# Performance work log

Measured on AMD Instinct MI355X. Metric: run time of the kernel, lower is better.

Reference implementation:

```python
import jax, jax.numpy as jnp
import numpy as np

BN_EPS = 1e-5


def setup_inputs() -> dict:
    key = jax.random.key(0)
    ks = jax.random.split(key, 5)
    b, c, seq, K = 16, 128, 16384, 64
    x = jax.random.normal(ks[0], (b, c, 1, seq), dtype=jnp.float32)
    std = 1.0 / np.sqrt(K * c)
    codewords = jax.random.uniform(ks[1], (K, c), dtype=jnp.float32, minval=-std, maxval=std)
    smoothing = jax.random.uniform(ks[2], (K,), dtype=jnp.float32, minval=-1.0, maxval=0.0)
    bn_weight = jnp.ones((K,), dtype=jnp.float32)
    bn_bias = jnp.zeros((K,), dtype=jnp.float32)
    fc_w = jax.random.normal(ks[3], (c, c), dtype=jnp.float32) * (1.0 / np.sqrt(c))
    fc_b = jax.random.uniform(ks[4], (c,), dtype=jnp.float32, minval=-1.0 / np.sqrt(c), maxval=1.0 / np.sqrt(c))
    return {"x": x, "codewords": codewords, "smoothing": smoothing,
            "bn_weight": bn_weight, "bn_bias": bn_bias, "fc_w": fc_w, "fc_b": fc_b}


def reference(x, codewords, smoothing, bn_weight, bn_bias, fc_w, fc_b):
    # x: (b, c, 1, seq); codewords: (K, c); smoothing: (K,)
    xs = jnp.transpose(x[:, :, 0, :], (0, 2, 1))          # (b, seq, c)
    # squared distances ||x - cw||^2 via expansion (avoids (b,seq,K,c) tensor)
    x2 = jnp.sum(xs * xs, axis=-1)                         # (b, seq)
    cw2 = jnp.sum(codewords * codewords, axis=-1)          # (K,)
    cross = jnp.einsum('bsc,kc->bsk', xs, codewords)       # (b, seq, K)
    d2 = x2[:, :, None] - 2.0 * cross + cw2[None, None, :]
    a = jax.nn.softmax(smoothing[None, None, :] * d2, axis=2)  # (b, seq, K)
    # e = sum_s a * (x - cw)  (residual aggregation, expansion-free)
    e = jnp.einsum('bsk,bsc->bkc', a, xs) - jnp.sum(a, axis=1)[:, :, None] * codewords[None]  # (b, K, c)
    # BatchNorm1d over K features (training-mode batch stats over dims (b, c))
    mean = jnp.mean(e, axis=(0, 2), keepdims=True)
    var = jnp.var(e, axis=(0, 2), keepdims=True)
    e_bn = (e - mean) / jnp.sqrt(var + BN_EPS) * bn_weight[None, :, None] + bn_bias[None, :, None]
    e_norm = jnp.mean(jax.nn.relu(e_bn), axis=1)           # (b, c)
    scale = jax.nn.sigmoid(e_norm @ fc_w.T + fc_b)         # (b, c)
    return x * scale[:, :, None, None]
```

## Files before the change

kernel.cpp:

```cpp
#include <hip/hip_runtime.h>

typedef unsigned int u32;
typedef unsigned short u16;
typedef unsigned long long u64;

typedef float f32x4 __attribute__((ext_vector_type(4)));
typedef short bf16x8 __attribute__((ext_vector_type(8)));

#define B_   16
#define C_   128
#define SEQ_ 16384
#define K_   64
#define TS_  64
#define NT_  8
#define CHUNK_ 512

constexpr int OFF_EACC = 0;
constexpr int OFF_ASUM = 131072;
constexpr int OFF_BNS  = 132096;
constexpr int OFF_BNB  = 132160;
constexpr int OFF_SM   = 136192;
constexpr int OFF_SMC2 = 136256;
constexpr int OFF_SCALE= 136320;

__device__ __forceinline__ u16 f2bf(float f) {
    u32 b = __float_as_uint(f);
    return (u16)((b + 0x7FFFu + ((b >> 16) & 1u)) >> 16);
}
__device__ __forceinline__ float scrub(float v) {
    return fminf(fmaxf(v, -1.0e4f), 1.0e4f);
}

__global__ void k0_prep(const float* __restrict__ cw, const float* __restrict__ sm,
                        float* __restrict__ ws) {
    const int t = threadIdx.x;
    if (t < K_) {
        float s2 = 0.f;
        for (int c = 0; c < C_; ++c) { float f = cw[t * C_ + c]; s2 += f * f; }
        float smv = sm[t];
        ws[OFF_SM + t] = smv;
        ws[OFF_SMC2 + t] = smv * s2;
    }
}

__global__ __launch_bounds__(256, 3)
void k1_encode(const float* __restrict__ xg, const float* __restrict__ cwg, float* ws) {
    __shared__ __align__(16) u16 xsc_h[TS_ * C_];
    __shared__ __align__(16) u16 xsc_l[TS_ * C_];
    __shared__ __align__(16) u16 alds[K_ * TS_];

    const int t    = threadIdx.x;
    const int lane = t & 63;
    const int w    = t >> 6;
    const int lk   = lane & 15;
    const int lg   = lane >> 4;
    const int b      = blockIdx.x >> 5;
    const int s_base = (blockIdx.x & 31) * CHUNK_;

    bf16x8 cwf[4][4];
#pragma unroll
    for (int nt = 0; nt < 4; ++nt)
#pragma unroll
      for (int ks = 0; ks < 4; ++ks) {
        const float* p = cwg + (size_t)(lk + 16*nt) * C_ + 8*lg + 32*ks;
        float4 v0 = *(const float4*)p;
        float4 v1 = *(const float4*)(p + 4);
        bf16x8 f;
        f[0]=(short)f2bf(v0.x); f[1]=(short)f2bf(v0.y); f[2]=(short)f2bf(v0.z); f[3]=(short)f2bf(v0.w);
        f[4]=(short)f2bf(v1.x); f[5]=(short)f2bf(v1.y); f[6]=(short)f2bf(v1.z); f[7]=(short)f2bf(v1.w);
        cwf[nt][ks] = f;
      }
    float smk[4], smc2k[4];
#pragma unroll
    for (int nt = 0; nt < 4; ++nt) {
        smk[nt]   = ws[OFF_SM   + lk + 16*nt];
        smc2k[nt] = ws[OFF_SMC2 + lk + 16*nt];
    }

    f32x4 acc2[4][2] = {};
    float asacc[4] = {0.f,0.f,0.f,0.f};

    const int sm_ = t & 15;
    const int sg_ = t >> 4;

    auto gemm2 = [&](int stp) {
#pragma unroll
        for (int ss = 0; ss < 2; ++ss) {
            bf16x8 aA[4];
#pragma unroll
            for (int mt = 0; mt < 4; ++mt)
                aA[mt] = *(const bf16x8*)&alds[(lk + 16*mt) * TS_ + ((8*lg + 32*ss) ^ ((lk & 7) << 3))];
#pragma unroll
            for (int n = 0; n < 2; ++n) {
                const float* xr = xg + (size_t)(b * C_ + lk + 16*(2*w + n)) * SEQ_ + stp + 8*lg + 32*ss;
                float4 v0 = *(const float4*)xr;
                float4 v1 = *(const float4*)(xr + 4);
                bf16x8 bx;
                ((u32*)&bx)[0] = (__float_as_uint(v0.x) >> 16) | (__float_as_uint(v0.y) & 0xFFFF0000u);
                ((u32*)&bx)[1] = (__float_as_uint(v0.z) >> 16) | (__float_as_uint(v0.w) & 0xFFFF0000u);
                ((u32*)&bx)[2] = (__float_as_uint(v1.x) >> 16) | (__float_as_uint(v1.y) & 0xFFFF0000u);
                ((u32*)&bx)[3] = (__float_as_uint(v1.z) >> 16) | (__float_as_uint(v1.w) & 0xFFFF0000u);
#pragma unroll
                for (int mt = 0; mt < 4; ++mt)
                    acc2[mt][n] = __builtin_amdgcn_mfma_f32_16x16x32_bf16(aA[mt], bx, acc2[mt][n], 0, 0, 0);
            }
        }
    };

    float4 vc[8];
    {
        const float* xb = xg + (size_t)(b * C_ + 8*sm_) * SEQ_ + s_base + 4*sg_;
#pragma unroll
        for (int r = 0; r < 8; ++r) vc[r] = *(const float4*)(xb + (size_t)r * SEQ_);
    }

    float x2red[4];

    for (int tile = 0; tile < NT_; ++tile) {
        const int st = s_base + tile * TS_;
        __syncthreads();

        {
            u16 H[8][4], L[8][4];
            float x2p[4] = {0.f,0.f,0.f,0.f};
#pragma unroll
            for (int r = 0; r < 8; ++r) {
                float fa[4] = {vc[r].x, vc[r].y, vc[r].z, vc[r].w};
#pragma unroll
                for (int i = 0; i < 4; ++i) {
                    float f = fa[i];
                    u32 bu = __float_as_uint(f);
                    u16 hh = (u16)(bu >> 16);
                    float fh = __uint_as_float((u32)hh << 16);
                    u16 ll = (u16)(__float_as_uint(f - fh) >> 16);
                    H[r][i] = hh; L[r][i] = ll;
                    x2p[i] = fmaf(f, f, x2p[i]);
                }
            }
            if (tile + 1 < NT_) {
                const float* xb = xg + (size_t)(b * C_ + 8*sm_) * SEQ_ + (st + TS_) + 4*sg_;
#pragma unroll
                for (int r = 0; r < 8; ++r) vc[r] = *(const float4*)(xb + (size_t)r * SEQ_);
            }
#pragma unroll
            for (int i = 0; i < 4; ++i) {
                float v = x2p[i];
                v += __shfl_xor(v, 1);
                v += __shfl_xor(v, 2);
                v += __shfl_xor(v, 4);
                v += __shfl_xor(v, 8);
                x2red[i] = v;
            }
#pragma unroll
            for (int i = 0; i < 4; ++i) {
                int s = 4*sg_ + i;
                u32 idx = (u32)(s * C_ + 8*sm_) ^ ((u32)(s & 15) << 3);
                uint4 hw, lw;
                hw.x = (u32)H[0][i] | ((u32)H[1][i] << 16);
                hw.y = (u32)H[2][i] | ((u32)H[3][i] << 16);
                hw.z = (u32)H[4][i] | ((u32)H[5][i] << 16);
                hw.w = (u32)H[6][i] | ((u32)H[7][i] << 16);
                lw.x = (u32)L[0][i] | ((u32)L[1][i] << 16);
                lw.y = (u32)L[2][i] | ((u32)L[3][i] << 16);
                lw.z = (u32)L[4][i] | ((u32)L[5][i] << 16);
                lw.w = (u32)L[6][i] | ((u32)L[7][i] << 16);
                *(uint4*)&xsc_h[idx] = hw;
                *(uint4*)&xsc_l[idx] = lw;
            }
        }
        if (tile > 0) gemm2(st - TS_);
        __syncthreads();

        f32x4 d1[4] = {};
        {
            const int sA = 16*w + lk;
#pragma unroll
            for (int ks = 0; ks < 4; ++ks) {
                u32 idx = (u32)(sA * C_ + 8*lg + 32*ks) ^ ((u32)(sA & 15) << 3);
                bf16x8 ah = *(const bf16x8*)&xsc_h[idx];
                bf16x8 al = *(const bf16x8*)&xsc_l[idx];
#pragma unroll
                for (int nt = 0; nt < 4; ++nt) {
                    d1[nt] = __builtin_amdgcn_mfma_f32_16x16x32_bf16(ah, cwf[nt][ks], d1[nt], 0, 0, 0);
                    d1[nt] = __builtin_amdgcn_mfma_f32_16x16x32_bf16(al, cwf[nt][ks], d1[nt], 0, 0, 0);
                }
            }
        }

        {
            float mx[4], pp[4][4], inv[4];
#pragma unroll
            for (int r = 0; r < 4; ++r) mx[r] = -1.0e30f;
#pragma unroll
            for (int nt = 0; nt < 4; ++nt)
#pragma unroll
              for (int r = 0; r < 4; ++r) {
                float lv = fmaf(smk[nt], x2red[r] - 2.0f * d1[nt][r], smc2k[nt]);
                lv = scrub(lv);
                pp[nt][r] = lv;
                mx[r] = fmaxf(mx[r], lv);
              }
#pragma unroll
            for (int r = 0; r < 4; ++r) {
                mx[r] = fmaxf(mx[r], __shfl_xor(mx[r], 1));
                mx[r] = fmaxf(mx[r], __shfl_xor(mx[r], 2));
                mx[r] = fmaxf(mx[r], __shfl_xor(mx[r], 4));
                mx[r] = fmaxf(mx[r], __shfl_xor(mx[r], 8));
            }
            float sum[4] = {0.f,0.f,0.f,0.f};
#pragma unroll
            for (int nt = 0; nt < 4; ++nt)
#pragma unroll
              for (int r = 0; r < 4; ++r) {
                float e = __expf(pp[nt][r] - mx[r]);
                pp[nt][r] = e;
                sum[r] += e;
              }
#pragma unroll
            for (int r = 0; r < 4; ++r) {
                sum[r] += __shfl_xor(sum[r], 1);
                sum[r] += __shfl_xor(sum[r], 2);
                sum[r] += __shfl_xor(sum[r], 4);
                sum[r] += __shfl_xor(sum[r], 8);
                inv[r] = 1.0f / sum[r];
            }
#pragma unroll
            for (int nt = 0; nt < 4; ++nt) {
                u16 q[4];
                float sloc = 0.f;
#pragma unroll
                for (int r = 0; r < 4; ++r) {
                    float a = pp[nt][r] * inv[r];
                    sloc += a;
                    q[r] = f2bf(a);
                }
                asacc[nt] += sloc;
                u64 pk = (u64)q[0] | ((u64)q[1] << 16) | ((u64)q[2] << 32) | ((u64)q[3] << 48);
                *(u64*)&alds[(lk + 16*nt) * TS_ + (((u32)(16*w + 4*lg)) ^ ((u32)(lk & 7) << 3))] = pk;
            }
        }
    }
    __syncthreads();
    gemm2(s_base + (NT_ - 1) * TS_);

    float* eacc = ws + OFF_EACC;
#pragma unroll
    for (int mt = 0; mt < 4; ++mt)
#pragma unroll
      for (int n = 0; n < 2; ++n) {
        const int c = lk + 16*(2*w + n);
#pragma unroll
        for (int r = 0; r < 4; ++r) {
            int k = 16*mt + 4*lg + r;
            atomicAdd(&eacc[(b * K_ + k) * C_ + c], acc2[mt][n][r]);
        }
      }
#pragma unroll
    for (int nt = 0; nt < 4; ++nt) {
        float v = asacc[nt];
        v += __shfl_xor(v, 16);
        v += __shfl_xor(v, 32);
        if (lane < 16) atomicAdd(&ws[OFF_ASUM + b * K_ + lk + 16*nt], v);
    }
}

__global__ __launch_bounds__(256)
void k2a_stats(const float* __restrict__ cw,
               const float* __restrict__ bnw, const float* __restrict__ bnb,
               float* ws) {
    const int k = blockIdx.x;
    const int t = threadIdx.x;
    const int lane = t & 63, w = t >> 6;
    __shared__ float redS[4], redQ[4];
    const float* eacc = ws + OFF_EACC;
    const float* asum = ws + OFF_ASUM;
    float sv = 0.f, sq = 0.f;
#pragma unroll
    for (int u = t; u < 512; u += 256) {
        int bb = u >> 5, c4 = u & 31;
        float a = asum[bb * K_ + k];
        float4 ev = *(const float4*)&eacc[(bb * K_ + k) * C_ + 4*c4];
        float4 cv = *(const float4*)&cw[k * C_ + 4*c4];
        float e0 = ev.x - a * cv.x, e1 = ev.y - a * cv.y;
        float e2 = ev.z - a * cv.z, e3 = ev.w - a * cv.w;
        sv += e0 + e1 + e2 + e3;
        sq += e0*e0 + e1*e1 + e2*e2 + e3*e3;
    }
#pragma unroll
    for (int m = 1; m < 64; m <<= 1) {
        sv += __shfl_xor(sv, m);
        sq += __shfl_xor(sq, m);
    }
    if (lane == 0) { redS[w] = sv; redQ[w] = sq; }
    __syncthreads();
    if (t == 0) {
        float s = redS[0]+redS[1]+redS[2]+redS[3];
        float q = redQ[0]+redQ[1]+redQ[2]+redQ[3];
        float mean = s * (1.f / 2048.f);
        float var  = q * (1.f / 2048.f) - mean * mean;
        float rstd = rsqrtf(fmaxf(var, 0.f) + 1e-5f);
        float g = bnw[k] * rstd;
        ws[OFF_BNS + k] = g;
        ws[OFF_BNB + k] = bnb[k] - mean * g;
    }
}

__global__ __launch_bounds__(256)
void k2b_fc(const float* __restrict__ cw,
            const float* __restrict__ fcw, const float* __restrict__ fcb,
            float* ws) {
    __shared__ float enorm_s[C_];
    __shared__ float red2[C_];
    const int b = blockIdx.x;
    const int t = threadIdx.x;
    const int c = t & 127, h = t >> 7;
    const float* eacc = ws + OFF_EACC;
    float s = 0.f;
    for (int kk = 0; kk < 32; ++kk) {
        int k = 32*h + kk;
        float e = eacc[(b * K_ + k) * C_ + c] - ws[OFF_ASUM + b * K_ + k] * cw[k * C_ + c];
        float bnv = e * ws[OFF_BNS + k] + ws[OFF_BNB + k];
        s += fminf(fmaxf(bnv, 0.f), 1.0e6f);
    }
    if (h) red2[c] = s;
    __syncthreads();
    if (!h) enorm_s[c] = (s + red2[c]) * (1.f / 64.f);
    __syncthreads();
    float acc = 0.f;
    const float4* fw = (const float4*)&fcw[c * C_ + 64*h];
#pragma unroll
    for (int q = 0; q < 16; ++q) {
        float4 wv = fw[q];
        int ci = 64*h + 4*q;
        acc += enorm_s[ci] * wv.x + enorm_s[ci+1] * wv.y + enorm_s[ci+2] * wv.z + enorm_s[ci+3] * wv.w;
    }
    __syncthreads();
    if (h) red2[c] = acc;
    __syncthreads();
    if (!h) {
        float o = fcb[c] + acc + red2[c];
        ws[OFF_SCALE + b * C_ + c] = 1.f / (1.f + __expf(-o));
    }
}

__global__ __launch_bounds__(256)
void k3_scale(const float4* __restrict__ xg, float4* __restrict__ outg,
              const float* __restrict__ ws) {
    const int bc = blockIdx.x;
    const float sc = ws[OFF_SCALE + bc];
    const float4* xr = xg + (size_t)bc * (SEQ_ / 4);
    float4* orow = outg + (size_t)bc * (SEQ_ / 4);
    const int t = threadIdx.x;
    for (int i = 0; i < SEQ_ / 4 / 256; ++i) {
        float4 v = xr[i * 256 + t];
        v.x *= sc; v.y *= sc; v.z *= sc; v.w *= sc;
        orow[i * 256 + t] = v;
    }
}

extern "C" void kernel_launch(void* const* d_in, const int* in_sizes, int n_in,
                              void* d_out, int out_size, void* d_ws, size_t ws_size,
                              hipStream_t stream) {
    const float* x   = (const float*)d_in[0];
    const float* cw  = (const float*)d_in[1];
    const float* sm  = (const float*)d_in[2];
    const float* bnw = (const float*)d_in[3];
    const float* bnb = (const float*)d_in[4];
    const float* fcw = (const float*)d_in[5];
    const float* fcb = (const float*)d_in[6];
    float* ws = (float*)d_ws;

    hipMemsetAsync(ws, 0, (size_t)(OFF_ASUM + B_ * K_) * sizeof(float), stream);
    k0_prep<<<1, 256, 0, stream>>>(cw, sm, ws);
    k1_encode<<<B_ * (SEQ_ / CHUNK_), 256, 0, stream>>>(x, cw, ws);
    k2a_stats<<<K_, 256, 0, stream>>>(cw, bnw, bnb, ws);
    k2b_fc<<<B_, 256, 0, stream>>>(cw, fcw, fcb, ws);
    k3_scale<<<B_ * C_, 256, 0, stream>>>((const float4*)x, (float4*)d_out, ws);
}
```

Baseline: 386.9 us.

## Fold codeword prep into encode kernel, halve chunk size, use perm packing

Removes the separate single-block prep kernel by computing codeword squared norms inside each encode block via shuffles, which drops one launch and its serialization. The per-block sequence chunk is halved, doubling the grid to 1024 blocks for better CU fill, and launch bounds drop from 3 to 2 waves per SIMD. The bf16 hi/lo splitting and packing now use byte-perm instructions and pack pairs directly instead of via intermediate u16 arrays. The trade-offs are redundant norm computation in every block, more atomic partial-sum traffic from the extra blocks, and possibly lower occupancy.

```diff
diff --git a/kernel.cpp b/kernel.cpp
--- a/kernel.cpp
+++ b/kernel.cpp
@@ -12,15 +12,13 @@
 #define SEQ_ 16384
 #define K_   64
 #define TS_  64
-#define NT_  8
-#define CHUNK_ 512
+#define NT_  4
+#define CHUNK_ 256
 
 constexpr int OFF_EACC = 0;
 constexpr int OFF_ASUM = 131072;
 constexpr int OFF_BNS  = 132096;
 constexpr int OFF_BNB  = 132160;
-constexpr int OFF_SM   = 136192;
-constexpr int OFF_SMC2 = 136256;
 constexpr int OFF_SCALE= 136320;
 
 __device__ __forceinline__ u16 f2bf(float f) {
@@ -30,21 +28,13 @@
 __device__ __forceinline__ float scrub(float v) {
     return fminf(fmaxf(v, -1.0e4f), 1.0e4f);
 }
-
-__global__ void k0_prep(const float* __restrict__ cw, const float* __restrict__ sm,
-                        float* __restrict__ ws) {
-    const int t = threadIdx.x;
-    if (t < K_) {
-        float s2 = 0.f;
-        for (int c = 0; c < C_; ++c) { float f = cw[t * C_ + c]; s2 += f * f; }
-        float smv = sm[t];
-        ws[OFF_SM + t] = smv;
-        ws[OFF_SMC2 + t] = smv * s2;
-    }
-}
-
-__global__ __launch_bounds__(256, 3)
-void k1_encode(const float* __restrict__ xg, const float* __restrict__ cwg, float* ws) {
+__device__ __forceinline__ u32 packhi(float f1, float f0) {
+    return __builtin_amdgcn_perm(__float_as_uint(f1), __float_as_uint(f0), 0x07060302u);
+}
+
+__global__ __launch_bounds__(256, 2)
+void k1_encode(const float* __restrict__ xg, const float* __restrict__ cwg,
+               const float* __restrict__ smg, float* ws) {
     __shared__ __align__(16) u16 xsc_h[TS_ * C_];
     __shared__ __align__(16) u16 xsc_l[TS_ * C_];
     __shared__ __align__(16) u16 alds[K_ * TS_];
@@ -54,10 +44,11 @@
     const int w    = t >> 6;
     const int lk   = lane & 15;
     const int lg   = lane >> 4;
-    const int b      = blockIdx.x >> 5;
-    const int s_base = (blockIdx.x & 31) * CHUNK_;
+    const int b      = blockIdx.x >> 6;
+    const int s_base = (blockIdx.x & 63) * CHUNK_;
 
     bf16x8 cwf[4][4];
+    float s2acc[4] = {0.f, 0.f, 0.f, 0.f};
 #pragma unroll
     for (int nt = 0; nt < 4; ++nt)
 #pragma unroll
@@ -65,6 +56,8 @@
         const float* p = cwg + (size_t)(lk + 16*nt) * C_ + 8*lg + 32*ks;
         float4 v0 = *(const float4*)p;
         float4 v1 = *(const float4*)(p + 4);
+        s2acc[nt] += v0.x*v0.x + v0.y*v0.y + v0.z*v0.z + v0.w*v0.w
+                   + v1.x*v1.x + v1.y*v1.y + v1.z*v1.z + v1.w*v1.w;
         bf16x8 f;
         f[0]=(short)f2bf(v0.x); f[1]=(short)f2bf(v0.y); f[2]=(short)f2bf(v0.z); f[3]=(short)f2bf(v0.w);
         f[4]=(short)f2bf(v1.x); f[5]=(short)f2bf(v1.y); f[6]=(short)f2bf(v1.z); f[7]=(short)f2bf(v1.w);
@@ -73,8 +66,11 @@
     float smk[4], smc2k[4];
 #pragma unroll
     for (int nt = 0; nt < 4; ++nt) {
-        smk[nt]   = ws[OFF_SM   + lk + 16*nt];
-        smc2k[nt] = ws[OFF_SMC2 + lk + 16*nt];
+        float s2 = s2acc[nt];
+        s2 += __shfl_xor(s2, 16);
+        s2 += __shfl_xor(s2, 32);
+        smk[nt]   = smg[lk + 16*nt];
+        smc2k[nt] = smk[nt] * s2;
     }
 
     f32x4 acc2[4][2] = {};
@@ -96,10 +92,10 @@
                 float4 v0 = *(const float4*)xr;
                 float4 v1 = *(const float4*)(xr + 4);
                 bf16x8 bx;
-                ((u32*)&bx)[0] = (__float_as_uint(v0.x) >> 16) | (__float_as_uint(v0.y) & 0xFFFF0000u);
-                ((u32*)&bx)[1] = (__float_as_uint(v0.z) >> 16) | (__float_as_uint(v0.w) & 0xFFFF0000u);
-                ((u32*)&bx)[2] = (__float_as_uint(v1.x) >> 16) | (__float_as_uint(v1.y) & 0xFFFF0000u);
-                ((u32*)&bx)[3] = (__float_as_uint(v1.z) >> 16) | (__float_as_uint(v1.w) & 0xFFFF0000u);
+                ((u32*)&bx)[0] = packhi(v0.y, v0.x);
+                ((u32*)&bx)[1] = packhi(v0.w, v0.z);
+                ((u32*)&bx)[2] = packhi(v1.y, v1.x);
+                ((u32*)&bx)[3] = packhi(v1.w, v1.z);
 #pragma unroll
                 for (int mt = 0; mt < 4; ++mt)
                     acc2[mt][n] = __builtin_amdgcn_mfma_f32_16x16x32_bf16(aA[mt], bx, acc2[mt][n], 0, 0, 0);
@@ -121,20 +117,22 @@
         __syncthreads();
 
         {
-            u16 H[8][4], L[8][4];
             float x2p[4] = {0.f,0.f,0.f,0.f};
-#pragma unroll
-            for (int r = 0; r < 8; ++r) {
-                float fa[4] = {vc[r].x, vc[r].y, vc[r].z, vc[r].w};
+            u32 hw[4][4], lw[4][4];
+#pragma unroll
+            for (int rp = 0; rp < 4; ++rp) {
+                float4 f0 = vc[2*rp], f1 = vc[2*rp + 1];
+                float fa0[4] = {f0.x, f0.y, f0.z, f0.w};
+                float fa1[4] = {f1.x, f1.y, f1.z, f1.w};
 #pragma unroll
                 for (int i = 0; i < 4; ++i) {
-                    float f = fa[i];
-                    u32 bu = __float_as_uint(f);
-                    u16 hh = (u16)(bu >> 16);
-                    float fh = __uint_as_float((u32)hh << 16);
-                    u16 ll = (u16)(__float_as_uint(f - fh) >> 16);
-                    H[r][i] = hh; L[r][i] = ll;
-                    x2p[i] = fmaf(f, f, x2p[i]);
+                    float a0 = fa0[i], a1 = fa1[i];
+                    hw[i][rp] = packhi(a1, a0);
+                    float h0 = __uint_as_float(__float_as_uint(a0) & 0xFFFF0000u);
+                    float h1 = __uint_as_float(__float_as_uint(a1) & 0xFFFF0000u);
+                    lw[i][rp] = packhi(a1 - h1, a0 - h0);
+                    x2p[i] = fmaf(a0, a0, x2p[i]);
+                    x2p[i] = fmaf(a1, a1, x2p[i]);
                 }
             }
             if (tile + 1 < NT_) {
@@ -155,17 +153,8 @@
             for (int i = 0; i < 4; ++i) {
                 int s = 4*sg_ + i;
                 u32 idx = (u32)(s * C_ + 8*sm_) ^ ((u32)(s & 15) << 3);
-                uint4 hw, lw;
-                hw.x = (u32)H[0][i] | ((u32)H[1][i] << 16);
-                hw.y = (u32)H[2][i] | ((u32)H[3][i] << 16);
-                hw.z = (u32)H[4][i] | ((u32)H[5][i] << 16);
-                hw.w = (u32)H[6][i] | ((u32)H[7][i] << 16);
-                lw.x = (u32)L[0][i] | ((u32)L[1][i] << 16);
-                lw.y = (u32)L[2][i] | ((u32)L[3][i] << 16);
-                lw.z = (u32)L[4][i] | ((u32)L[5][i] << 16);
-                lw.w = (u32)L[6][i] | ((u32)L[7][i] << 16);
-                *(uint4*)&xsc_h[idx] = hw;
-                *(uint4*)&xsc_l[idx] = lw;
+                *(uint4*)&xsc_h[idx] = make_uint4(hw[i][0], hw[i][1], hw[i][2], hw[i][3]);
+                *(uint4*)&xsc_l[idx] = make_uint4(lw[i][0], lw[i][1], lw[i][2], lw[i][3]);
             }
         }
         if (tile > 0) gemm2(st - TS_);
@@ -371,8 +360,7 @@
     float* ws = (float*)d_ws;
 
     hipMemsetAsync(ws, 0, (size_t)(OFF_ASUM + B_ * K_) * sizeof(float), stream);
-    k0_prep<<<1, 256, 0, stream>>>(cw, sm, ws);
-    k1_encode<<<B_ * (SEQ_ / CHUNK_), 256, 0, stream>>>(x, cw, ws);
+    k1_encode<<<B_ * (SEQ_ / CHUNK_), 256, 0, stream>>>(x, cw, sm, ws);
     k2a_stats<<<K_, 256, 0, stream>>>(cw, bnw, bnb, ws);
     k2b_fc<<<B_, 256, 0, stream>>>(cw, fcw, fcb, ws);
     k3_scale<<<B_ * C_, 256, 0, stream>>>((const float4*)x, (float4*)d_out, ws);
```

Result: faster. 322.9 us (-16.5%).
